# Optimization experiments

Measured on AMD Instinct MI355X. Metric: run time of the kernel, lower is better.

Reference implementation:

```python
import jax, jax.numpy as jnp
import numpy as np

# Multi-scale feature pyramid (H, W) per level: strides 8/16/32/64 on a ~512px image
SHAPES = ((64, 64), (32, 32), (16, 16), (8, 8))
N_HEADS, N_LEVELS, N_POINTS = 8, 4, 4
D_MODEL = 256
HEAD_DIM = D_MODEL // N_HEADS


def setup_inputs() -> dict:
    key = jax.random.key(0)
    ks = jax.random.split(key, 11)
    B, C = 4, D_MODEL
    Lv = sum(h * w for h, w in SHAPES)  # 5440
    Lq = Lv  # encoder self-attention: queries are the flattened features
    scale = 0.02
    return {
        "query": jax.random.normal(ks[0], (B, Lq, C), jnp.float32),
        "reference_points": jax.random.uniform(ks[1], (B, Lq, N_LEVELS, 2), jnp.float32),
        "value": jax.random.normal(ks[2], (B, Lv, C), jnp.float32),
        "W_off": jax.random.normal(ks[3], (C, N_HEADS * N_LEVELS * N_POINTS * 2), jnp.float32) * scale,
        "b_off": jax.random.normal(ks[4], (N_HEADS * N_LEVELS * N_POINTS * 2,), jnp.float32) * 0.5,
        "W_attn": jax.random.normal(ks[5], (C, N_HEADS * N_LEVELS * N_POINTS), jnp.float32) * scale,
        "b_attn": jax.random.normal(ks[6], (N_HEADS * N_LEVELS * N_POINTS,), jnp.float32) * scale,
        "W_val": jax.random.normal(ks[7], (C, C), jnp.float32) * scale,
        "b_val": jax.random.normal(ks[8], (C,), jnp.float32) * scale,
        "W_out": jax.random.normal(ks[9], (C, C), jnp.float32) * scale,
        "b_out": jax.random.normal(ks[10], (C,), jnp.float32) * scale,
    }


def _bilinear_sample(val, grid, H, W):
    """Replicates F.grid_sample(mode='bilinear', padding_mode='zeros', align_corners=False).

    val:  [N, C, H, W]
    grid: [N, Lq, P, 2] in [-1, 1] (x, y order)
    returns: [N, C, Lq, P]
    """
    N, C = val.shape[0], val.shape[1]
    # unnormalize (align_corners=False)
    x = (grid[..., 0] + 1.0) * 0.5 * W - 0.5  # [N, Lq, P]
    y = (grid[..., 1] + 1.0) * 0.5 * H - 0.5
    x0 = jnp.floor(x)
    y0 = jnp.floor(y)
    wx = x - x0  # fractional parts
    wy = y - y0
    flat = val.reshape(N, C, H * W)

    def gather(xi, yi):
        valid = (xi >= 0) & (xi < W) & (yi >= 0) & (yi < H)
        xc = jnp.clip(xi, 0, W - 1).astype(jnp.int32)
        yc = jnp.clip(yi, 0, H - 1).astype(jnp.int32)
        idx = yc * W + xc  # [N, Lq, P]
        g = jax.vmap(lambda v, i: v[:, i])(flat, idx)  # [N, C, Lq, P]
        return g * valid[:, None, :, :].astype(val.dtype)

    out = (gather(x0, y0) * ((1 - wx) * (1 - wy))[:, None]
           + gather(x0 + 1, y0) * (wx * (1 - wy))[:, None]
           + gather(x0, y0 + 1) * ((1 - wx) * wy)[:, None]
           + gather(x0 + 1, y0 + 1) * (wx * wy)[:, None])
    return out


def _ms_deform_attn(query, reference_points, value, W_off, b_off, W_attn, b_attn,
                    W_val, b_val, W_out, b_out):
    B, Lq, C = query.shape
    val = value @ W_val + b_val  # [B, Lv, C]
    val = val.reshape(B, -1, N_HEADS, HEAD_DIM)

    offsets = (query @ W_off + b_off).reshape(B, Lq, N_HEADS, N_LEVELS, N_POINTS, 2)
    weights = jax.nn.softmax(
        (query @ W_attn + b_attn).reshape(B, Lq, N_HEADS, N_LEVELS * N_POINTS), axis=-1
    ).reshape(B, Lq, N_HEADS, N_LEVELS, N_POINTS)

    # offset normalizer: (W, H) per level
    offset_norm = jnp.array([[w, h] for h, w in SHAPES], jnp.float32)
    # ref_dim == 2 branch
    locs = reference_points[:, :, None, :, None, :] + offsets / offset_norm[None, None, None, :, None, :]
    grids = 2.0 * locs - 1.0  # [B, Lq, nh, nl, np, 2]

    acc = jnp.zeros((B * N_HEADS, HEAD_DIM, Lq), query.dtype)
    start = 0
    for lid, (H, W) in enumerate(SHAPES):
        # [B, HW, nh, hd] -> [B*nh, hd, H, W]
        v = val[:, start:start + H * W].transpose(0, 2, 3, 1).reshape(B * N_HEADS, HEAD_DIM, H, W)
        g = grids[:, :, :, lid].transpose(0, 2, 1, 3, 4).reshape(B * N_HEADS, Lq, N_POINTS, 2)
        s = _bilinear_sample(v, g, H, W)  # [B*nh, hd, Lq, np]
        w = weights[:, :, :, lid].transpose(0, 2, 1, 3).reshape(B * N_HEADS, 1, Lq, N_POINTS)
        acc = acc + (s * w).sum(-1)
        start += H * W

    out = acc.reshape(B, D_MODEL, Lq).transpose(0, 2, 1)  # [B, Lq, C]
    return out @ W_out + b_out


def reference(query, reference_points, value, W_off, b_off, W_attn, b_attn,
              W_val, b_val, W_out, b_out):
    return _ms_deform_attn(query, reference_points, value, W_off, b_off,
                           W_attn, b_attn, W_val, b_val, W_out, b_out)
```

## Files before the change

### kernel.cpp

```cpp
#include <hip/hip_runtime.h>


typedef __attribute__((ext_vector_type(8))) _Float16 half8;
typedef __attribute__((ext_vector_type(4))) float f32x4;

typedef __attribute__((address_space(3))) unsigned int lds_uint;
typedef const __attribute__((address_space(1))) unsigned int g_uint;

__device__ __forceinline__ void load_lds16(const _Float16* g, _Float16* l) {
    __builtin_amdgcn_global_load_lds((g_uint*)g, (lds_uint*)l, 16, 0, 0);
}

__device__ __forceinline__ half8 splat8(_Float16 v) {
    half8 r = {v, v, v, v, v, v, v, v};
    return r;
}

#define M_TOTAL 21760

__global__ __launch_bounds__(256, 4) void gemm12_cvt(
    const float* __restrict__ value, const float* __restrict__ query,
    const float* __restrict__ W_val, const float* __restrict__ W_off,
    const float* __restrict__ W_attn,
    const float* __restrict__ b_val, const float* __restrict__ b_off,
    const float* __restrict__ b_attn,
    _Float16* __restrict__ valh, _Float16* __restrict__ offh)
{
    __shared__ _Float16 Af[2][4 * 64 * 8];
    __shared__ _Float16 Bf[2][4 * 128 * 8];

    const bool g1 = blockIdx.x < 680;
    const int id = g1 ? blockIdx.x : blockIdx.x - 680;
    const int mt = g1 ? (id >> 1) : (id / 3);
    const int nt = g1 ? (id & 1) : (id % 3);
    const int NN = g1 ? 256 : 384;
    const float* A = g1 ? value : query;
    _Float16* C = g1 ? valh : offh;
    const int bm = mt * 64;
    const int bn = nt * 128;

    const float* W;
    int sW, nb;
    if (g1)            { W = W_val;  sW = 256; nb = bn; }
    else if (nt < 2)   { W = W_off;  sW = 256; nb = bn; }
    else               { W = W_attn; sW = 128; nb = 0;  }

    const int tid = threadIdx.x;
    const int wave = tid >> 6, lane = tid & 63;
    const int wm = (wave & 1) * 32, wn = (wave >> 1) * 64;
    const int ml = lane & 15;
    const int gq = lane >> 4;

    const int ar = tid & 63,  ag = tid >> 6;
    const int bc = tid & 127, bh = tid >> 7;

    const float* aS = A + (size_t)(bm + ar) * 256 + ag * 8;
    const float* wS = W + (size_t)(bh * 16) * sW + nb + bc;

    float4 pa0, pa1;
    float pb[16];

    auto LOAD = [&](int kt) {
        const float* p = aS + kt * 32;
        pa0 = *(const float4*)(p + 0);
        pa1 = *(const float4*)(p + 4);
        const float* q = wS + (size_t)kt * 32 * sW;
#pragma unroll
        for (int e = 0; e < 16; ++e) pb[e] = q[(size_t)e * sW];
    };

    auto WRITE = [&](int buf) {
        const half8 ha = {(_Float16)pa0.x, (_Float16)pa0.y, (_Float16)pa0.z, (_Float16)pa0.w,
                          (_Float16)pa1.x, (_Float16)pa1.y, (_Float16)pa1.z, (_Float16)pa1.w};
        const half8 hb0 = {(_Float16)pb[0], (_Float16)pb[1], (_Float16)pb[2], (_Float16)pb[3],
                           (_Float16)pb[4], (_Float16)pb[5], (_Float16)pb[6], (_Float16)pb[7]};
        const half8 hb1 = {(_Float16)pb[8], (_Float16)pb[9], (_Float16)pb[10], (_Float16)pb[11],
                           (_Float16)pb[12], (_Float16)pb[13], (_Float16)pb[14], (_Float16)pb[15]};
        *(half8*)(&Af[buf][0] + ((ag * 64 + ar) << 3)) = ha;
        *(half8*)(&Bf[buf][0] + (((bh * 2) * 128 + bc) << 3)) = hb0;
        *(half8*)(&Bf[buf][0] + (((bh * 2 + 1) * 128 + bc) << 3)) = hb1;
    };

    const f32x4 zero4 = {0.f, 0.f, 0.f, 0.f};
    f32x4 acc[2][4];
#pragma unroll
    for (int i = 0; i < 2; ++i)
#pragma unroll
        for (int j = 0; j < 4; ++j) acc[i][j] = zero4;

    LOAD(0);
    int cur = 0;
    for (int kt = 0; kt < 8; ++kt) {
        WRITE(cur);
        if (kt < 7) LOAD(kt + 1);
        __syncthreads();

        half8 af[2], bf[4];
        const _Float16* ab = &Af[cur][0] + ((size_t)gq * 64 << 3);
        const _Float16* bb = &Bf[cur][0] + ((size_t)gq * 128 << 3);
#pragma unroll
        for (int i = 0; i < 2; ++i)
            af[i] = *(const half8*)(ab + ((wm + i * 16 + ml) << 3));
#pragma unroll
        for (int j = 0; j < 4; ++j)
            bf[j] = *(const half8*)(bb + ((wn + j * 16 + ml) << 3));
#pragma unroll
        for (int i = 0; i < 2; ++i)
#pragma unroll
            for (int j = 0; j < 4; ++j)
                acc[i][j] = __builtin_amdgcn_mfma_f32_16x16x32_f16(af[i], bf[j], acc[i][j], 0, 0, 0);
        cur ^= 1;
    }

    const int r0 = (lane >> 4) * 4;
#pragma unroll
    for (int j = 0; j < 4; ++j) {
        const int col = bn + wn + j * 16 + ml;
        const float bj = g1 ? b_val[col] : (col < 256 ? b_off[col] : b_attn[col - 256]);
#pragma unroll
        for (int i = 0; i < 2; ++i) {
            const size_t rbase = (size_t)(bm + wm + i * 16 + r0) * NN + col;
#pragma unroll
            for (int r = 0; r < 4; ++r)
                C[rbase + (size_t)r * NN] = (_Float16)(acc[i][j][r] + bj);
        }
    }
}

__device__ __forceinline__ void gemm_core(
    const _Float16* __restrict__ A, const _Float16* __restrict__ Bt,
    const float* __restrict__ bias, float* __restrict__ Cv,
    int NN, int mt, int nt)
{
    __shared__ _Float16 Ah[128 * 32];
    __shared__ _Float16 Bh[64 * 32];

    const int tid = threadIdx.x;
    const int bm = mt * 128;
    const int bn = nt * 64;
    const int wave = tid >> 6, lane = tid & 63;
    const int wm = (wave & 1) * 64, wn = (wave >> 1) * 32;
    const int ml = lane & 15, kq = (lane >> 4) * 8;
    const int lr = lane >> 2;
    const int lk = (lane & 3) * 8;

    const f32x4 zero4 = {0.f, 0.f, 0.f, 0.f};
    f32x4 acc[4][2];
#pragma unroll
    for (int i = 0; i < 4; ++i)
#pragma unroll
        for (int j = 0; j < 2; ++j) acc[i][j] = zero4;

    for (int kt = 0; kt < 8; ++kt) {
        const int k0 = kt * 32;
        __syncthreads();
#pragma unroll
        for (int t = 0; t < 2; ++t) {
            const int row = wave * 32 + t * 16;
            load_lds16(A + (size_t)(bm + row + lr) * 256 + k0 + lk,
                       Ah + (size_t)row * 32);
        }
        {
            const int row = wave * 16;
            load_lds16(Bt + (size_t)(bn + row + lr) * 256 + k0 + lk,
                       Bh + (size_t)row * 32);
        }
        __syncthreads();

        half8 af[4], bf[2];
#pragma unroll
        for (int i = 0; i < 4; ++i)
            af[i] = *(const half8*)(Ah + (wm + i * 16 + ml) * 32 + kq);
#pragma unroll
        for (int j = 0; j < 2; ++j)
            bf[j] = *(const half8*)(Bh + (wn + j * 16 + ml) * 32 + kq);
#pragma unroll
        for (int i = 0; i < 4; ++i)
#pragma unroll
            for (int j = 0; j < 2; ++j)
                acc[i][j] = __builtin_amdgcn_mfma_f32_16x16x32_f16(af[i], bf[j], acc[i][j], 0, 0, 0);
    }

    const int r0 = (lane >> 4) * 4;
#pragma unroll
    for (int j = 0; j < 2; ++j) {
        const int col = bn + wn + j * 16 + ml;
        const float bj = bias[col];
#pragma unroll
        for (int i = 0; i < 4; ++i) {
            const size_t rbase = (size_t)(bm + wm + i * 16 + r0) * NN + col;
#pragma unroll
            for (int r = 0; r < 4; ++r)
                Cv[rbase + (size_t)r * NN] = acc[i][j][r] + bj;
        }
    }
}

__global__ __launch_bounds__(256) void gemm_single(
    const _Float16* __restrict__ A, const _Float16* __restrict__ Bt,
    const float* __restrict__ bias, float* __restrict__ Cv)
{
    const int id = blockIdx.x;
    gemm_core(A, Bt, bias, Cv, 256, id >> 2, id & 3);
}

__global__ __launch_bounds__(256, 4) void sample_f16(
    const _Float16* __restrict__ valh,
    const float* __restrict__ refp,
    const _Float16* __restrict__ offh,
    const float* __restrict__ W_out,
    _Float16* __restrict__ wto,
    _Float16* __restrict__ acc_out)
{
    if (blockIdx.x < 256)
        wto[blockIdx.x * 256 + threadIdx.x] =
            (_Float16)W_out[threadIdx.x * 256 + blockIdx.x];

    const int wave = threadIdx.x >> 6, lane = threadIdx.x & 63;
    const int q2 = lane >> 5, sl = lane & 31;
    const int bq = blockIdx.x * 8 + wave * 2 + q2;
    const int b = bq / 5440;
    const int h = sl >> 2;
    const int d8 = (sl & 3) * 8;

    const _Float16* off_row = offh + (size_t)bq * 384 + h * 32;
    const _Float16* att_row = offh + (size_t)bq * 384 + 256 + h * 16;
    const float* rp = refp + (size_t)bq * 8;

    const half8 ofr0 = *(const half8*)(off_row);
    const half8 ofr1 = *(const half8*)(off_row + 8);
    const half8 ofr2 = *(const half8*)(off_row + 16);
    const half8 ofr3 = *(const half8*)(off_row + 24);
    float lg[16];
    {
        const half8 t0 = *(const half8*)(att_row);
        const half8 t1 = *(const half8*)(att_row + 8);
#pragma unroll
        for (int j = 0; j < 8; ++j) { lg[j] = (float)t0[j]; lg[8 + j] = (float)t1[j]; }
    }
    float mx = -1e30f;
#pragma unroll
    for (int i = 0; i < 16; ++i) mx = fmaxf(mx, lg[i]);
    float s = 0.f;
#pragma unroll
    for (int i = 0; i < 16; ++i) { lg[i] = __expf(lg[i] - mx); s += lg[i]; }
    const float inv = 1.f / s;

    const float4 rp01 = *(const float4*)rp;
    const float4 rp23 = *(const float4*)(rp + 4);
    const float rxs[4] = {rp01.x, rp01.z, rp23.x, rp23.z};
    const float rys[4] = {rp01.y, rp01.w, rp23.y, rp23.w};

    const int Ws_[4] = {64, 32, 16, 8};
    const int starts_[4] = {0, 4096, 5120, 5376};

    half8 acc = splat8((_Float16)0.f);
#pragma unroll
    for (int l = 0; l < 4; ++l) {
        const int W = Ws_[l];
        const float fW = (float)W;
        const _Float16* vbase = valh + ((size_t)(b * 5440 + starts_[l])) * 256 + h * 32 + d8;
        const float rx = rxs[l], ry = rys[l];

        int idx_[16];
        _Float16 w_[16];
#pragma unroll
        for (int p = 0; p < 4; ++p) {
            const int pi = l * 4 + p;
            const float aw = lg[pi] * inv;
            float ox, oy;
            {
                const half8 src = (pi < 8) ? ((pi < 4) ? ofr0 : ofr1)
                                           : ((pi < 12) ? ofr2 : ofr3);
                const int e = (pi & 3) * 2;
                ox = (float)src[e];
                oy = (float)src[e + 1];
            }
            const float x = fmaf(rx, fW, ox) - 0.5f;
            const float y = fmaf(ry, fW, oy) - 0.5f;
            const float x0f = floorf(x), y0f = floorf(y);
            const int x0 = (int)x0f, y0 = (int)y0f;
            const float wx = x - x0f, wy = y - y0f;
            const bool okx0 = ((unsigned)x0 < (unsigned)W);
            const bool okx1 = ((unsigned)(x0 + 1) < (unsigned)W);
            const bool oky0 = ((unsigned)y0 < (unsigned)W);
            const bool oky1 = ((unsigned)(y0 + 1) < (unsigned)W);
            const int xc0 = min(max(x0, 0), W - 1);
            const int xc1 = min(max(x0 + 1, 0), W - 1);
            const int yc0 = min(max(y0, 0), W - 1);
            const int yc1 = min(max(y0 + 1, 0), W - 1);
            w_[p * 4 + 0] = (_Float16)((okx0 & oky0) ? (1.f - wx) * (1.f - wy) * aw : 0.f);
            w_[p * 4 + 1] = (_Float16)((okx1 & oky0) ? wx * (1.f - wy) * aw : 0.f);
            w_[p * 4 + 2] = (_Float16)((okx0 & oky1) ? (1.f - wx) * wy * aw : 0.f);
            w_[p * 4 + 3] = (_Float16)((okx1 & oky1) ? wx * wy * aw : 0.f);
            idx_[p * 4 + 0] = (yc0 * W + xc0) * 256;
            idx_[p * 4 + 1] = (yc0 * W + xc1) * 256;
            idx_[p * 4 + 2] = (yc1 * W + xc0) * 256;
            idx_[p * 4 + 3] = (yc1 * W + xc1) * 256;
        }

        __builtin_amdgcn_sched_barrier(0);
        half8 c_[16];
#pragma unroll
        for (int i = 0; i < 16; ++i)
            c_[i] = *(const half8*)(vbase + idx_[i]);
        __builtin_amdgcn_sched_barrier(0);
#pragma unroll
        for (int i = 0; i < 16; ++i)
            acc += c_[i] * splat8(w_[i]);
    }

    *(half8*)(acc_out + (size_t)bq * 256 + h * 32 + d8) = acc;
}

extern "C" void kernel_launch(void* const* d_in, const int* in_sizes, int n_in,
                              void* d_out, int out_size, void* d_ws, size_t ws_size,
                              hipStream_t stream) {
    const float* query  = (const float*)d_in[0];
    const float* refp   = (const float*)d_in[1];
    const float* value  = (const float*)d_in[2];
    const float* W_off  = (const float*)d_in[3];
    const float* b_off  = (const float*)d_in[4];
    const float* W_attn = (const float*)d_in[5];
    const float* b_attn = (const float*)d_in[6];
    const float* W_val  = (const float*)d_in[7];
    const float* b_val  = (const float*)d_in[8];
    const float* W_out  = (const float*)d_in[9];
    const float* b_out  = (const float*)d_in[10];
    float* out = (float*)d_out;

    const size_t M = M_TOTAL;

    _Float16* valh  = (_Float16*)d_ws;
    _Float16* offh  = valh + M * 256;
    _Float16* acc16 = offh + M * 384;
    _Float16* wto   = acc16 + M * 256;

    dim3 blk(256);
    gemm12_cvt<<<dim3(1700), blk, 0, stream>>>(
        value, query, W_val, W_off, W_attn, b_val, b_off, b_attn, valh, offh);
    sample_f16<<<dim3(M / 8), blk, 0, stream>>>(valh, refp, offh, W_out, wto, acc16);
    gemm_single<<<dim3(680), blk, 0, stream>>>(acc16, wto, b_out, out);
}
```

Baseline: 176.3 us.

## Split sampling-coordinate math across lanes and broadcast packed index/weight via shuffles

Before, each of the four lanes sharing a head computed bilinear indices and weights for all 16 level/point pairs redundantly. Now each lane handles one level: it loads only that level's offsets, logits and reference point, does a cross-lane softmax with xor shuffles, and packs each 16-bit index and fp16 weight into one 32-bit word. During the gather loop these words are broadcast with __shfl from the lane owning each level. This cuts redundant ALU work and loads by about four times, at the cost of 64 shuffles per thread and the packing and unpacking.

```diff
diff --git a/kernel.cpp b/kernel.cpp
--- a/kernel.cpp
+++ b/kernel.cpp
@@ -2,6 +2,7 @@
 
 
 typedef __attribute__((ext_vector_type(8))) _Float16 half8;
+typedef __attribute__((ext_vector_type(4))) _Float16 half4;
 typedef __attribute__((ext_vector_type(4))) float f32x4;
 
 typedef __attribute__((address_space(3))) unsigned int lds_uint;
@@ -221,93 +222,86 @@
     const int bq = blockIdx.x * 8 + wave * 2 + q2;
     const int b = bq / 5440;
     const int h = sl >> 2;
-    const int d8 = (sl & 3) * 8;
-
-    const _Float16* off_row = offh + (size_t)bq * 384 + h * 32;
-    const _Float16* att_row = offh + (size_t)bq * 384 + 256 + h * 16;
-    const float* rp = refp + (size_t)bq * 8;
-
-    const half8 ofr0 = *(const half8*)(off_row);
-    const half8 ofr1 = *(const half8*)(off_row + 8);
-    const half8 ofr2 = *(const half8*)(off_row + 16);
-    const half8 ofr3 = *(const half8*)(off_row + 24);
-    float lg[16];
-    {
-        const half8 t0 = *(const half8*)(att_row);
-        const half8 t1 = *(const half8*)(att_row + 8);
-#pragma unroll
-        for (int j = 0; j < 8; ++j) { lg[j] = (float)t0[j]; lg[8 + j] = (float)t1[j]; }
-    }
-    float mx = -1e30f;
-#pragma unroll
-    for (int i = 0; i < 16; ++i) mx = fmaxf(mx, lg[i]);
+    const int t = sl & 3;
+    const int d8 = t * 8;
+
+    const int Wt = 64 >> t;
+    const float fW = (float)Wt;
+
+    const half8 ofr = *(const half8*)(offh + (size_t)bq * 384 + h * 32 + t * 8);
+    const half4 lgt = *(const half4*)(offh + (size_t)bq * 384 + 256 + h * 16 + t * 4);
+    const float2 rxy = *(const float2*)(refp + (size_t)bq * 8 + t * 2);
+
+    float lg[4];
+#pragma unroll
+    for (int p = 0; p < 4; ++p) lg[p] = (float)lgt[p];
+
+    float mx = fmaxf(fmaxf(lg[0], lg[1]), fmaxf(lg[2], lg[3]));
+    mx = fmaxf(mx, __shfl_xor(mx, 1));
+    mx = fmaxf(mx, __shfl_xor(mx, 2));
     float s = 0.f;
 #pragma unroll
-    for (int i = 0; i < 16; ++i) { lg[i] = __expf(lg[i] - mx); s += lg[i]; }
+    for (int p = 0; p < 4; ++p) { lg[p] = __expf(lg[p] - mx); s += lg[p]; }
+    s += __shfl_xor(s, 1);
+    s += __shfl_xor(s, 2);
     const float inv = 1.f / s;
 
-    const float4 rp01 = *(const float4*)rp;
-    const float4 rp23 = *(const float4*)(rp + 4);
-    const float rxs[4] = {rp01.x, rp01.z, rp23.x, rp23.z};
-    const float rys[4] = {rp01.y, rp01.w, rp23.y, rp23.w};
-
-    const int Ws_[4] = {64, 32, 16, 8};
+    unsigned pk[16];
+#pragma unroll
+    for (int p = 0; p < 4; ++p) {
+        const float aw = lg[p] * inv;
+        const float ox = (float)ofr[p * 2];
+        const float oy = (float)ofr[p * 2 + 1];
+        const float x = fmaf(rxy.x, fW, ox) - 0.5f;
+        const float y = fmaf(rxy.y, fW, oy) - 0.5f;
+        const float x0f = floorf(x), y0f = floorf(y);
+        const int x0 = (int)x0f, y0 = (int)y0f;
+        const float wx = x - x0f, wy = y - y0f;
+        const bool okx0 = ((unsigned)x0 < (unsigned)Wt);
+        const bool okx1 = ((unsigned)(x0 + 1) < (unsigned)Wt);
+        const bool oky0 = ((unsigned)y0 < (unsigned)Wt);
+        const bool oky1 = ((unsigned)(y0 + 1) < (unsigned)Wt);
+        const int xc0 = min(max(x0, 0), Wt - 1);
+        const int xc1 = min(max(x0 + 1, 0), Wt - 1);
+        const int yc0 = min(max(y0, 0), Wt - 1);
+        const int yc1 = min(max(y0 + 1, 0), Wt - 1);
+        const _Float16 w0 = (_Float16)((okx0 & oky0) ? (1.f - wx) * (1.f - wy) * aw : 0.f);
+        const _Float16 w1 = (_Float16)((okx1 & oky0) ? wx * (1.f - wy) * aw : 0.f);
+        const _Float16 w2 = (_Float16)((okx0 & oky1) ? (1.f - wx) * wy * aw : 0.f);
+        const _Float16 w3 = (_Float16)((okx1 & oky1) ? wx * wy * aw : 0.f);
+        pk[p * 4 + 0] = ((unsigned)(yc0 * Wt + xc0) << 16) |
+                        (unsigned)__builtin_bit_cast(unsigned short, w0);
+        pk[p * 4 + 1] = ((unsigned)(yc0 * Wt + xc1) << 16) |
+                        (unsigned)__builtin_bit_cast(unsigned short, w1);
+        pk[p * 4 + 2] = ((unsigned)(yc1 * Wt + xc0) << 16) |
+                        (unsigned)__builtin_bit_cast(unsigned short, w2);
+        pk[p * 4 + 3] = ((unsigned)(yc1 * Wt + xc1) << 16) |
+                        (unsigned)__builtin_bit_cast(unsigned short, w3);
+    }
+
     const int starts_[4] = {0, 4096, 5120, 5376};
+    const int gbase = lane & ~3;
 
     half8 acc = splat8((_Float16)0.f);
 #pragma unroll
     for (int l = 0; l < 4; ++l) {
-        const int W = Ws_[l];
-        const float fW = (float)W;
         const _Float16* vbase = valh + ((size_t)(b * 5440 + starts_[l])) * 256 + h * 32 + d8;
-        const float rx = rxs[l], ry = rys[l];
-
-        int idx_[16];
-        _Float16 w_[16];
-#pragma unroll
-        for (int p = 0; p < 4; ++p) {
-            const int pi = l * 4 + p;
-            const float aw = lg[pi] * inv;
-            float ox, oy;
-            {
-                const half8 src = (pi < 8) ? ((pi < 4) ? ofr0 : ofr1)
-                                           : ((pi < 12) ? ofr2 : ofr3);
-                const int e = (pi & 3) * 2;
-                ox = (float)src[e];
-                oy = (float)src[e + 1];
-            }
-            const float x = fmaf(rx, fW, ox) - 0.5f;
-            const float y = fmaf(ry, fW, oy) - 0.5f;
-            const float x0f = floorf(x), y0f = floorf(y);
-            const int x0 = (int)x0f, y0 = (int)y0f;
-            const float wx = x - x0f, wy = y - y0f;
-            const bool okx0 = ((unsigned)x0 < (unsigned)W);
-            const bool okx1 = ((unsigned)(x0 + 1) < (unsigned)W);
-            const bool oky0 = ((unsigned)y0 < (unsigned)W);
-            const bool oky1 = ((unsigned)(y0 + 1) < (unsigned)W);
-            const int xc0 = min(max(x0, 0), W - 1);
-            const int xc1 = min(max(x0 + 1, 0), W - 1);
-            const int yc0 = min(max(y0, 0), W - 1);
-            const int yc1 = min(max(y0 + 1, 0), W - 1);
-            w_[p * 4 + 0] = (_Float16)((okx0 & oky0) ? (1.f - wx) * (1.f - wy) * aw : 0.f);
-            w_[p * 4 + 1] = (_Float16)((okx1 & oky0) ? wx * (1.f - wy) * aw : 0.f);
-            w_[p * 4 + 2] = (_Float16)((okx0 & oky1) ? (1.f - wx) * wy * aw : 0.f);
-            w_[p * 4 + 3] = (_Float16)((okx1 & oky1) ? wx * wy * aw : 0.f);
-            idx_[p * 4 + 0] = (yc0 * W + xc0) * 256;
-            idx_[p * 4 + 1] = (yc0 * W + xc1) * 256;
-            idx_[p * 4 + 2] = (yc1 * W + xc0) * 256;
-            idx_[p * 4 + 3] = (yc1 * W + xc1) * 256;
-        }
+        const int src = gbase + l;
+
+        unsigned q_[16];
+#pragma unroll
+        for (int c = 0; c < 16; ++c)
+            q_[c] = (unsigned)__shfl((int)pk[c], src);
 
         __builtin_amdgcn_sched_barrier(0);
         half8 c_[16];
 #pragma unroll
-        for (int i = 0; i < 16; ++i)
-            c_[i] = *(const half8*)(vbase + idx_[i]);
+        for (int c = 0; c < 16; ++c)
+            c_[c] = *(const half8*)(vbase + ((size_t)(q_[c] >> 16) << 8));
         __builtin_amdgcn_sched_barrier(0);
 #pragma unroll
-        for (int i = 0; i < 16; ++i)
-            acc += c_[i] * splat8(w_[i]);
+        for (int c = 0; c < 16; ++c)
+            acc += c_[c] * splat8(__builtin_bit_cast(_Float16, (unsigned short)(q_[c] & 0xffffu)));
     }
 
     *(half8*)(acc_out + (size_t)bq * 256 + h * 32 + d8) = acc;
```

Measured after the change: 172.9 us. No clear change (-1.9%).
